# Performance work log

Hardware: AMD Instinct MI355X
Metric: run time of the kernel (lower is better)

The kernel has to match this reference:

```python
import jax, jax.numpy as jnp
import numpy as np

N = 8388608  # flattened batch*seq tokens
C = 2        # binary classification, per source


def setup_inputs() -> dict:
    key = jax.random.key(0)
    k1, k2 = jax.random.split(key)
    x = jax.random.normal(k1, (N, C), dtype=jnp.float32)
    targets = jax.random.randint(k2, (N,), 0, 2, dtype=jnp.int64)
    return {"x": x, "targets": targets}


def reference(x, targets):
    # log-softmax over classes
    logs = jax.nn.log_softmax(x, axis=1)  # [N, C]
    # gather log-prob at the target class per sample
    picked = jnp.take_along_axis(logs, targets[:, None].astype(jnp.int32), axis=1)[:, 0]  # [N]
    is_one = (targets == 1)
    is_zero = (targets == 0)
    n_one = jnp.sum(is_one)
    n_zero = jnp.sum(is_zero)
    sum_one = jnp.sum(jnp.where(is_one, picked, 0.0))
    sum_zero = jnp.sum(jnp.where(is_zero, picked, 0.0))
    # class-conditional mean of -log p; 0 if the class is absent
    r = jnp.where(n_one > 0, -sum_one / jnp.maximum(n_one, 1), 0.0)
    p = jnp.where(n_zero > 0, -sum_zero / jnp.maximum(n_zero, 1), 0.0)
    return p + r
```

## Files before the change

### kernel.cpp

```cpp
#include <hip/hip_runtime.h>

#define BLOCK 256
#define NBLOCKS 2048
#define BLOCK2 1024

__global__ __launch_bounds__(BLOCK) void nll_partial(
    const float4* __restrict__ x4,
    const int4* __restrict__ t4,
    float* __restrict__ ps0,
    float* __restrict__ ps1,
    unsigned int* __restrict__ pc1,
    int nquads)
{
    int idx = blockIdx.x * blockDim.x + threadIdx.x;
    int stride = gridDim.x * blockDim.x;

    float s0 = 0.f, s1 = 0.f;
    unsigned int c1 = 0;

    for (int i = idx; i < nquads; i += stride) {
        float4 xa = x4[2 * i];
        float4 xb = x4[2 * i + 1];
        int4   t  = t4[i];

        float a, b, m, lse;

        a = xa.x; b = xa.y;
        m = fmaxf(a, b);
        lse = m + __logf(__expf(a - m) + __expf(b - m));
        s1 += t.x ? (lse - b) : 0.f;
        s0 += t.x ? 0.f : (lse - a);
        c1 += (t.x != 0);

        a = xa.z; b = xa.w;
        m = fmaxf(a, b);
        lse = m + __logf(__expf(a - m) + __expf(b - m));
        s1 += t.y ? (lse - b) : 0.f;
        s0 += t.y ? 0.f : (lse - a);
        c1 += (t.y != 0);

        a = xb.x; b = xb.y;
        m = fmaxf(a, b);
        lse = m + __logf(__expf(a - m) + __expf(b - m));
        s1 += t.z ? (lse - b) : 0.f;
        s0 += t.z ? 0.f : (lse - a);
        c1 += (t.z != 0);

        a = xb.z; b = xb.w;
        m = fmaxf(a, b);
        lse = m + __logf(__expf(a - m) + __expf(b - m));
        s1 += t.w ? (lse - b) : 0.f;
        s0 += t.w ? 0.f : (lse - a);
        c1 += (t.w != 0);
    }

    for (int off = 32; off > 0; off >>= 1) {
        s0 += __shfl_down(s0, off, 64);
        s1 += __shfl_down(s1, off, 64);
        c1 += __shfl_down(c1, off, 64);
    }

    __shared__ float sh0[BLOCK / 64];
    __shared__ float sh1[BLOCK / 64];
    __shared__ unsigned int shc[BLOCK / 64];

    int lane = threadIdx.x & 63;
    int wave = threadIdx.x >> 6;
    if (lane == 0) { sh0[wave] = s0; sh1[wave] = s1; shc[wave] = c1; }
    __syncthreads();

    if (threadIdx.x == 0) {
        float t0 = 0.f, t1 = 0.f;
        unsigned int tc = 0;
        for (int w = 0; w < BLOCK / 64; ++w) { t0 += sh0[w]; t1 += sh1[w]; tc += shc[w]; }
        ps0[blockIdx.x] = t0;
        ps1[blockIdx.x] = t1;
        pc1[blockIdx.x] = tc;
    }
}

__global__ __launch_bounds__(BLOCK2) void nll_finalize(
    const float* __restrict__ ps0,
    const float* __restrict__ ps1,
    const unsigned int* __restrict__ pc1,
    const float* __restrict__ x,
    const int* __restrict__ tg,
    float* __restrict__ out,
    int P, int N, int tail_start)
{
    float s0 = 0.f, s1 = 0.f;
    unsigned int c1 = 0;
    for (int i = threadIdx.x; i < P; i += BLOCK2) {
        s0 += ps0[i];
        s1 += ps1[i];
        c1 += pc1[i];
    }

    for (int off = 32; off > 0; off >>= 1) {
        s0 += __shfl_down(s0, off, 64);
        s1 += __shfl_down(s1, off, 64);
        c1 += __shfl_down(c1, off, 64);
    }

    __shared__ float sh0[BLOCK2 / 64];
    __shared__ float sh1[BLOCK2 / 64];
    __shared__ unsigned int shc[BLOCK2 / 64];

    int lane = threadIdx.x & 63;
    int wave = threadIdx.x >> 6;
    if (lane == 0) { sh0[wave] = s0; sh1[wave] = s1; shc[wave] = c1; }
    __syncthreads();

    if (threadIdx.x == 0) {
        float t0 = 0.f, t1 = 0.f;
        unsigned int tc = 0;
        for (int w = 0; w < BLOCK2 / 64; ++w) { t0 += sh0[w]; t1 += sh1[w]; tc += shc[w]; }
        for (int i = tail_start; i < N; ++i) {
            float a = x[2 * i], b = x[2 * i + 1];
            float m = fmaxf(a, b);
            float lse = m + __logf(__expf(a - m) + __expf(b - m));
            if (tg[i]) { t1 += lse - b; tc++; } else { t0 += lse - a; }
        }
        unsigned int c0 = (unsigned int)N - tc;
        float r = (tc > 0) ? t1 / (float)tc : 0.f;
        float p = (c0 > 0) ? t0 / (float)c0 : 0.f;
        out[0] = p + r;
    }
}

__global__ void nll_atomic(const float4* __restrict__ x4,
                           const int4* __restrict__ t4,
                           float* __restrict__ wsf,
                           unsigned int* __restrict__ wsi,
                           int nquads)
{
    int idx = blockIdx.x * blockDim.x + threadIdx.x;
    int stride = gridDim.x * blockDim.x;
    float s0 = 0.f, s1 = 0.f;
    unsigned int c1 = 0;
    for (int i = idx; i < nquads; i += stride) {
        float4 xa = x4[2 * i];
        float4 xb = x4[2 * i + 1];
        int4   t  = t4[i];
        float a, b, m, lse;
        a = xa.x; b = xa.y; m = fmaxf(a, b);
        lse = m + __logf(__expf(a - m) + __expf(b - m));
        s1 += t.x ? (lse - b) : 0.f; s0 += t.x ? 0.f : (lse - a); c1 += (t.x != 0);
        a = xa.z; b = xa.w; m = fmaxf(a, b);
        lse = m + __logf(__expf(a - m) + __expf(b - m));
        s1 += t.y ? (lse - b) : 0.f; s0 += t.y ? 0.f : (lse - a); c1 += (t.y != 0);
        a = xb.x; b = xb.y; m = fmaxf(a, b);
        lse = m + __logf(__expf(a - m) + __expf(b - m));
        s1 += t.z ? (lse - b) : 0.f; s0 += t.z ? 0.f : (lse - a); c1 += (t.z != 0);
        a = xb.z; b = xb.w; m = fmaxf(a, b);
        lse = m + __logf(__expf(a - m) + __expf(b - m));
        s1 += t.w ? (lse - b) : 0.f; s0 += t.w ? 0.f : (lse - a); c1 += (t.w != 0);
    }
    for (int off = 32; off > 0; off >>= 1) {
        s0 += __shfl_down(s0, off, 64);
        s1 += __shfl_down(s1, off, 64);
        c1 += __shfl_down(c1, off, 64);
    }
    __shared__ float sh0[4]; __shared__ float sh1[4]; __shared__ unsigned int shc[4];
    int lane = threadIdx.x & 63; int wave = threadIdx.x >> 6;
    if (lane == 0) { sh0[wave] = s0; sh1[wave] = s1; shc[wave] = c1; }
    __syncthreads();
    if (threadIdx.x == 0) {
        float t0 = 0.f, t1 = 0.f; unsigned int tc = 0;
        for (int w = 0; w < 4; ++w) { t0 += sh0[w]; t1 += sh1[w]; tc += shc[w]; }
        atomicAdd(&wsf[0], t0); atomicAdd(&wsf[1], t1); atomicAdd(&wsi[0], tc);
    }
}

__global__ void nll_atomic_fin(const float* __restrict__ x,
                               const int* __restrict__ tg,
                               const float* __restrict__ wsf,
                               const unsigned int* __restrict__ wsi,
                               float* __restrict__ out,
                               int N, int tail_start)
{
    float s0 = wsf[0], s1 = wsf[1];
    unsigned int c1 = wsi[0];
    for (int i = tail_start; i < N; ++i) {
        float a = x[2 * i], b = x[2 * i + 1];
        float m = fmaxf(a, b);
        float lse = m + __logf(__expf(a - m) + __expf(b - m));
        if (tg[i]) { s1 += lse - b; c1++; } else { s0 += lse - a; }
    }
    unsigned int c0 = (unsigned int)N - c1;
    float r = (c1 > 0) ? s1 / (float)c1 : 0.f;
    float p = (c0 > 0) ? s0 / (float)c0 : 0.f;
    out[0] = p + r;
}

extern "C" void kernel_launch(void* const* d_in, const int* in_sizes, int n_in,
                              void* d_out, int out_size, void* d_ws, size_t ws_size,
                              hipStream_t stream) {
    const float* x = (const float*)d_in[0];
    const int* tg = (const int*)d_in[1];
    int N = in_sizes[1];
    float* out = (float*)d_out;

    int nquads = N / 4;
    int tail_start = nquads * 4;

    size_t need = (size_t)NBLOCKS * (4 + 4 + 4);
    if (ws_size >= need) {
        float* ps0 = (float*)d_ws;
        float* ps1 = ps0 + NBLOCKS;
        unsigned int* pc1 = (unsigned int*)(ps1 + NBLOCKS);

        nll_partial<<<NBLOCKS, BLOCK, 0, stream>>>(
            (const float4*)x, (const int4*)tg, ps0, ps1, pc1, nquads);
        nll_finalize<<<1, BLOCK2, 0, stream>>>(
            ps0, ps1, pc1, x, tg, out, NBLOCKS, N, tail_start);
    } else {
        float* wsf = (float*)d_ws;
        unsigned int* wsi = (unsigned int*)((char*)d_ws + 8);
        hipMemsetAsync(d_ws, 0, 16, stream);
        int blocks = 256;
        nll_atomic<<<blocks, BLOCK, 0, stream>>>(
            (const float4*)x, (const int4*)tg, wsf, wsi, nquads);
        nll_atomic_fin<<<1, 1, 0, stream>>>(x, tg, wsf, wsi, out, N, tail_start);
    }
}
```

Before: 115.3 us.

## Fuse finalize into partial kernel via last-block atomic counter

Replaces the separate finalize kernel with a last-block-done pattern. Each block publishes its partial sums, bumps an agent-scope counter with acq_rel ordering, and the final block reduces all partials and writes the output. This removes one kernel launch and the gap between kernels, but adds a memset launch to reset the counter and an atomic per block.

```diff
diff --git a/kernel.cpp b/kernel.cpp
--- a/kernel.cpp
+++ b/kernel.cpp
@@ -2,15 +2,18 @@
 
 #define BLOCK 256
 #define NBLOCKS 2048
-#define BLOCK2 1024
-
-__global__ __launch_bounds__(BLOCK) void nll_partial(
+
+__global__ __launch_bounds__(BLOCK) void nll_fused(
     const float4* __restrict__ x4,
     const int4* __restrict__ t4,
     float* __restrict__ ps0,
     float* __restrict__ ps1,
     unsigned int* __restrict__ pc1,
-    int nquads)
+    unsigned int* __restrict__ counter,
+    const float* __restrict__ x,
+    const int* __restrict__ tg,
+    float* __restrict__ out,
+    int nquads, int N, int tail_start)
 {
     int idx = blockIdx.x * blockDim.x + threadIdx.x;
     int stride = gridDim.x * blockDim.x;
@@ -63,6 +66,7 @@
     __shared__ float sh0[BLOCK / 64];
     __shared__ float sh1[BLOCK / 64];
     __shared__ unsigned int shc[BLOCK / 64];
+    __shared__ bool amLast;
 
     int lane = threadIdx.x & 63;
     int wave = threadIdx.x >> 6;
@@ -73,58 +77,46 @@
         float t0 = 0.f, t1 = 0.f;
         unsigned int tc = 0;
         for (int w = 0; w < BLOCK / 64; ++w) { t0 += sh0[w]; t1 += sh1[w]; tc += shc[w]; }
-        ps0[blockIdx.x] = t0;
-        ps1[blockIdx.x] = t1;
-        pc1[blockIdx.x] = tc;
-    }
-}
-
-__global__ __launch_bounds__(BLOCK2) void nll_finalize(
-    const float* __restrict__ ps0,
-    const float* __restrict__ ps1,
-    const unsigned int* __restrict__ pc1,
-    const float* __restrict__ x,
-    const int* __restrict__ tg,
-    float* __restrict__ out,
-    int P, int N, int tail_start)
-{
-    float s0 = 0.f, s1 = 0.f;
-    unsigned int c1 = 0;
-    for (int i = threadIdx.x; i < P; i += BLOCK2) {
-        s0 += ps0[i];
-        s1 += ps1[i];
-        c1 += pc1[i];
-    }
-
-    for (int off = 32; off > 0; off >>= 1) {
-        s0 += __shfl_down(s0, off, 64);
-        s1 += __shfl_down(s1, off, 64);
-        c1 += __shfl_down(c1, off, 64);
-    }
-
-    __shared__ float sh0[BLOCK2 / 64];
-    __shared__ float sh1[BLOCK2 / 64];
-    __shared__ unsigned int shc[BLOCK2 / 64];
-
-    int lane = threadIdx.x & 63;
-    int wave = threadIdx.x >> 6;
-    if (lane == 0) { sh0[wave] = s0; sh1[wave] = s1; shc[wave] = c1; }
+        __hip_atomic_store(&ps0[blockIdx.x], t0, __ATOMIC_RELAXED, __HIP_MEMORY_SCOPE_AGENT);
+        __hip_atomic_store(&ps1[blockIdx.x], t1, __ATOMIC_RELAXED, __HIP_MEMORY_SCOPE_AGENT);
+        __hip_atomic_store(&pc1[blockIdx.x], tc, __ATOMIC_RELAXED, __HIP_MEMORY_SCOPE_AGENT);
+        unsigned int prev = __hip_atomic_fetch_add(counter, 1u, __ATOMIC_ACQ_REL,
+                                                   __HIP_MEMORY_SCOPE_AGENT);
+        amLast = (prev == (unsigned int)(gridDim.x - 1));
+    }
     __syncthreads();
 
-    if (threadIdx.x == 0) {
-        float t0 = 0.f, t1 = 0.f;
-        unsigned int tc = 0;
-        for (int w = 0; w < BLOCK2 / 64; ++w) { t0 += sh0[w]; t1 += sh1[w]; tc += shc[w]; }
-        for (int i = tail_start; i < N; ++i) {
-            float a = x[2 * i], b = x[2 * i + 1];
-            float m = fmaxf(a, b);
-            float lse = m + __logf(__expf(a - m) + __expf(b - m));
-            if (tg[i]) { t1 += lse - b; tc++; } else { t0 += lse - a; }
+    if (amLast) {
+        float f0 = 0.f, f1 = 0.f;
+        unsigned int fc = 0;
+        for (int i = threadIdx.x; i < NBLOCKS; i += BLOCK) {
+            f0 += __hip_atomic_load(&ps0[i], __ATOMIC_RELAXED, __HIP_MEMORY_SCOPE_AGENT);
+            f1 += __hip_atomic_load(&ps1[i], __ATOMIC_RELAXED, __HIP_MEMORY_SCOPE_AGENT);
+            fc += __hip_atomic_load(&pc1[i], __ATOMIC_RELAXED, __HIP_MEMORY_SCOPE_AGENT);
         }
-        unsigned int c0 = (unsigned int)N - tc;
-        float r = (tc > 0) ? t1 / (float)tc : 0.f;
-        float p = (c0 > 0) ? t0 / (float)c0 : 0.f;
-        out[0] = p + r;
+        for (int off = 32; off > 0; off >>= 1) {
+            f0 += __shfl_down(f0, off, 64);
+            f1 += __shfl_down(f1, off, 64);
+            fc += __shfl_down(fc, off, 64);
+        }
+        __syncthreads();
+        if (lane == 0) { sh0[wave] = f0; sh1[wave] = f1; shc[wave] = fc; }
+        __syncthreads();
+        if (threadIdx.x == 0) {
+            float t0 = 0.f, t1 = 0.f;
+            unsigned int tc = 0;
+            for (int w = 0; w < BLOCK / 64; ++w) { t0 += sh0[w]; t1 += sh1[w]; tc += shc[w]; }
+            for (int i = tail_start; i < N; ++i) {
+                float a = x[2 * i], b = x[2 * i + 1];
+                float m = fmaxf(a, b);
+                float lse = m + __logf(__expf(a - m) + __expf(b - m));
+                if (tg[i]) { t1 += lse - b; tc++; } else { t0 += lse - a; }
+            }
+            unsigned int c0 = (unsigned int)N - tc;
+            float r = (tc > 0) ? t1 / (float)tc : 0.f;
+            float p = (c0 > 0) ? t0 / (float)c0 : 0.f;
+            out[0] = p + r;
+        }
     }
 }
 
@@ -204,22 +196,22 @@
     int nquads = N / 4;
     int tail_start = nquads * 4;
 
-    size_t need = (size_t)NBLOCKS * (4 + 4 + 4);
+    size_t need = 16 + (size_t)NBLOCKS * 12;
     if (ws_size >= need) {
-        float* ps0 = (float*)d_ws;
+        unsigned int* counter = (unsigned int*)d_ws;
+        float* ps0 = (float*)((char*)d_ws + 16);
         float* ps1 = ps0 + NBLOCKS;
         unsigned int* pc1 = (unsigned int*)(ps1 + NBLOCKS);
 
-        nll_partial<<<NBLOCKS, BLOCK, 0, stream>>>(
-            (const float4*)x, (const int4*)tg, ps0, ps1, pc1, nquads);
-        nll_finalize<<<1, BLOCK2, 0, stream>>>(
-            ps0, ps1, pc1, x, tg, out, NBLOCKS, N, tail_start);
+        hipMemsetAsync(counter, 0, 4, stream);
+        nll_fused<<<NBLOCKS, BLOCK, 0, stream>>>(
+            (const float4*)x, (const int4*)tg, ps0, ps1, pc1, counter,
+            x, tg, out, nquads, N, tail_start);
     } else {
         float* wsf = (float*)d_ws;
         unsigned int* wsi = (unsigned int*)((char*)d_ws + 8);
         hipMemsetAsync(d_ws, 0, 16, stream);
-        int blocks = 256;
-        nll_atomic<<<blocks, BLOCK, 0, stream>>>(
+        nll_atomic<<<256, BLOCK, 0, stream>>>(
             (const float4*)x, (const int4*)tg, wsf, wsi, nquads);
         nll_atomic_fin<<<1, 1, 0, stream>>>(x, tg, wsf, wsi, out, N, tail_start);
     }
```

Measured after the change: 203.2 us. 1.76x slower.
